# Kernel tuning notes

Measured on AMD Instinct MI355X. Metric: run time of the kernel, lower is better.

## Reference

```python
import jax, jax.numpy as jnp
import numpy as np

EMB = 512
HEADS = 8

def setup_inputs() -> dict:
    key = jax.random.key(0)
    ks = jax.random.split(key, 6)
    x = jax.random.normal(ks[0], (8, 1024, EMB), dtype=jnp.float32)
    s = EMB ** -0.5
    Wq = jax.random.normal(ks[1], (EMB, EMB), dtype=jnp.float32) * s
    Wk = jax.random.normal(ks[2], (EMB, EMB), dtype=jnp.float32) * s
    Wv = jax.random.normal(ks[3], (EMB, EMB), dtype=jnp.float32) * s
    ln_gamma = jnp.ones((EMB,), dtype=jnp.float32)
    ln_beta = jnp.zeros((EMB,), dtype=jnp.float32)
    return {"x": x, "Wq": Wq, "Wk": Wk, "Wv": Wv, "ln_gamma": ln_gamma, "ln_beta": ln_beta}

def reference(x, Wq, Wk, Wv, ln_gamma, ln_beta):
    B, S, E = x.shape
    H = HEADS
    D = E // H
    scale = E ** -0.5  # note: source scales by emb_size**-0.5, not head_dim
    # projections (bias=False, torch Linear: x @ W.T)
    q = (x @ Wq.T).reshape(B, S, H, D).transpose(0, 2, 1, 3)  # [B,H,S,D]
    k = (x @ Wk.T).reshape(B, S, H, D).transpose(0, 2, 1, 3)
    v = (x @ Wv.T).reshape(B, S, H, D).transpose(0, 2, 1, 3)
    attn = jnp.einsum('bhqd,bhkd->bhqk', q, k) * scale
    attn = jax.nn.softmax(attn, axis=-1)
    out = jnp.einsum('bhqk,bhkd->bhqd', attn, v)
    out = out.transpose(0, 2, 1, 3).reshape(B, S, E)
    # LayerNorm (eps=1e-5, torch default)
    mu = jnp.mean(out, axis=-1, keepdims=True)
    var = jnp.var(out, axis=-1, keepdims=True)
    out = (out - mu) * jax.lax.rsqrt(var + 1e-5) * ln_gamma + ln_beta
    return out
```

## Files before the change

kernel.cpp:

```cpp
#include <hip/hip_runtime.h>
#include <hip/hip_bf16.h>

typedef __bf16 bf16_t;
typedef __bf16 bf16x4 __attribute__((ext_vector_type(4)));
typedef __bf16 bf16x8 __attribute__((ext_vector_type(8)));
typedef float  f32x4  __attribute__((ext_vector_type(4)));
typedef short  short4v __attribute__((ext_vector_type(4)));

#define GLL(gp, lp) __builtin_amdgcn_global_load_lds((const __attribute__((address_space(1))) void*)(gp), (__attribute__((address_space(3))) void*)(lp), 16, 0, 0)

__device__ __forceinline__ f32x4 mfma16x16x16_bf16(bf16x4 a, bf16x4 b, f32x4 c) {
#if __has_builtin(__builtin_amdgcn_mfma_f32_16x16x16_bf16)
    return __builtin_amdgcn_mfma_f32_16x16x16_bf16(a, b, c, 0, 0, 0);
#else
    return __builtin_amdgcn_mfma_f32_16x16x16bf16_1k(__builtin_bit_cast(short4v, a), __builtin_bit_cast(short4v, b), c, 0, 0, 0);
#endif
}

__global__ __launch_bounds__(256) void cvt_kernel(const float* __restrict__ x,
                                                  const float* __restrict__ wq,
                                                  const float* __restrict__ wk,
                                                  const float* __restrict__ wv,
                                                  bf16_t* __restrict__ xb,
                                                  bf16_t* __restrict__ wall) {
    const int TOT4 = 1245184;
    for (int i = blockIdx.x * blockDim.x + threadIdx.x; i < TOT4; i += gridDim.x * blockDim.x) {
        const float* src; bf16_t* dst; int off;
        if (i < 1048576) { src = x; dst = xb; off = i; }
        else {
            int j = i - 1048576;
            int wsel = j >> 16;
            off = j & 65535;
            src = (wsel == 0) ? wq : ((wsel == 1) ? wk : wv);
            dst = wall + ((size_t)wsel << 18);
        }
        float4 v = *(const float4*)(src + (size_t)off * 4);
        bf16x4 o = { (bf16_t)v.x, (bf16_t)v.y, (bf16_t)v.z, (bf16_t)v.w };
        *(bf16x4*)(dst + (size_t)off * 4) = o;
    }
}

__global__ __launch_bounds__(256) void proj_kernel(const bf16_t* __restrict__ xb,
                                                   const bf16_t* __restrict__ wall,
                                                   bf16_t* __restrict__ Qb,
                                                   bf16_t* __restrict__ Kb,
                                                   bf16_t* __restrict__ Vt) {
    __shared__ bf16_t smW[128 * 32];
    __shared__ bf16_t smX[128 * 32];
    __shared__ bf16_t ctile[128 * 136];

    const int tid = threadIdx.x;
    const int w = tid >> 6, lane = tid & 63;
    const int bx = blockIdx.x;
    const int nb = bx % 12, mb = bx / 12;
    const int n0 = nb * 128, m0 = mb * 128;
    const int wn = w & 1, wm = w >> 1;
    const int l15 = lane & 15, g = lane >> 4;

    const int srow = w * 32 + (lane >> 2);
    const int kcol = (lane & 3) * 8;
    const bf16_t* wsrc0 = wall + (size_t)(n0 + srow) * 512 + kcol;
    const bf16_t* xsrc0 = xb + (size_t)(m0 + srow) * 512 + kcol;
    bf16_t* lw = smW + w * 1024;
    bf16_t* lx = smX + w * 1024;

    f32x4 acc[4][4] = {};

    for (int kt = 0; kt < 16; ++kt) {
        const int ko = kt * 32;
        GLL(wsrc0 + ko, lw);
        GLL(wsrc0 + 16 * 512 + ko, lw + 512);
        GLL(xsrc0 + ko, lx);
        GLL(xsrc0 + 16 * 512 + ko, lx + 512);
        __syncthreads();

        bf16x8 af[4], bfv[4];
#pragma unroll
        for (int ni = 0; ni < 4; ++ni)
            af[ni] = *(const bf16x8*)(smW + (wn * 64 + ni * 16 + l15) * 32 + g * 8);
#pragma unroll
        for (int mi = 0; mi < 4; ++mi)
            bfv[mi] = *(const bf16x8*)(smX + (wm * 64 + mi * 16 + l15) * 32 + g * 8);
#pragma unroll
        for (int ni = 0; ni < 4; ++ni)
#pragma unroll
            for (int mi = 0; mi < 4; ++mi)
                acc[ni][mi] = __builtin_amdgcn_mfma_f32_16x16x32_bf16(af[ni], bfv[mi], acc[ni][mi], 0, 0, 0);
        __syncthreads();
    }

    const int which = n0 >> 9;
    if (which < 2) {
        bf16_t* dst = (which == 0) ? Qb : Kb;
#pragma unroll
        for (int ni = 0; ni < 4; ++ni) {
#pragma unroll
            for (int mi = 0; mi < 4; ++mi) {
                int j = (n0 & 511) + wn * 64 + ni * 16 + g * 4;
                int h = j >> 6, dd = j & 63;
                int sb = m0 + wm * 64 + mi * 16 + l15;
                int b = sb >> 10, s = sb & 1023;
                bf16x4 o = { (bf16_t)acc[ni][mi][0], (bf16_t)acc[ni][mi][1],
                             (bf16_t)acc[ni][mi][2], (bf16_t)acc[ni][mi][3] };
                *(bf16x4*)(dst + ((size_t)((b * 8 + h) * 1024 + s)) * 64 + dd) = o;
            }
        }
    } else {
#pragma unroll
        for (int ni = 0; ni < 4; ++ni)
#pragma unroll
            for (int mi = 0; mi < 4; ++mi)
#pragma unroll
                for (int r = 0; r < 4; ++r)
                    ctile[(wn * 64 + ni * 16 + g * 4 + r) * 136 + wm * 64 + mi * 16 + l15] =
                        (bf16_t)acc[ni][mi][r];
        __syncthreads();
        const int rr = tid >> 1, half = tid & 1;
        const int jv = (n0 & 511) + rr;
        const int hh = jv >> 6, dd = jv & 63;
        const int b = m0 >> 10, sb = (m0 & 1023) + half * 64;
        bf16_t* dst = Vt + ((size_t)((b * 8 + hh) * 64 + dd)) * 1024 + sb;
        const bf16_t* src = ctile + rr * 136 + half * 64;
#pragma unroll
        for (int u = 0; u < 8; ++u)
            *(bf16x8*)(dst + u * 8) = *(const bf16x8*)(src + u * 8);
    }
}

__global__ __launch_bounds__(256) void attn_kernel(const bf16_t* __restrict__ Qb,
                                                   const bf16_t* __restrict__ Kb,
                                                   const bf16_t* __restrict__ Vt,
                                                   bf16_t* __restrict__ Ob) {
    __shared__ char smem[32768];
    const int tid = threadIdx.x;
    const int w = tid >> 6, lane = tid & 63;
    const int l15 = lane & 15, g = lane >> 4, l7 = lane & 7;

    const int bx = blockIdx.x;
    const int xcd = bx & 7, i = bx >> 3;
    const int head = xcd * 8 + (i & 7);
    const int qblk = i >> 3;
    const int q0 = qblk * 128 + w * 32;

    const size_t hoff = (size_t)head << 16;
    const bf16_t* Qh = Qb + hoff;
    const char* Kh = (const char*)(Kb + hoff);
    const char* Vh = (const char*)(Vt + hoff);

    const float c2 = 0.06376390597f;

    bf16x8 qf[2][2];
#pragma unroll
    for (int qh = 0; qh < 2; ++qh) {
        const bf16_t* qp = Qh + (q0 + qh * 16 + l15) * 64 + g * 8;
        bf16x8 a = *(const bf16x8*)(qp);
        bf16x8 b = *(const bf16x8*)(qp + 32);
#pragma unroll
        for (int j = 0; j < 8; ++j) {
            a[j] = (bf16_t)((float)a[j] * c2);
            b[j] = (bf16_t)((float)b[j] * c2);
        }
        qf[qh][0] = a; qf[qh][1] = b;
    }

    const int srow = w * 8 + (lane >> 3);
    const int sw16 = (l7 ^ ((lane >> 3) & 7)) << 4;
    const char* Ksrc = Kh + srow * 128 + sw16;
    const char* Vsrc = Vh + srow * 2048 + sw16;
    char* dstK = smem + w * 1024;
    char* dstV = smem + 8192 + w * 1024;

    const int e0 = (l7 ^ g) << 4;
    const int f0 = (g << 3) ^ (l7 << 4);

    float m2[2] = { -1e30f, -1e30f };
    float denom[2] = { 0.f, 0.f };
    f32x4 oacc[2][4] = {};

    GLL(Ksrc, dstK);
    GLL(Ksrc + 4096, dstK + 4096);
    GLL(Vsrc, dstV);
    GLL(Vsrc + 65536, dstV + 4096);
    __syncthreads();

    for (int c = 0; c < 16; ++c) {
        const int buf = c & 1;
        if (c < 15) {
            const int nbo = (buf ^ 1) * 16384;
            GLL(Ksrc + (c + 1) * 8192, dstK + nbo);
            GLL(Ksrc + (c + 1) * 8192 + 4096, dstK + nbo + 4096);
            GLL(Vsrc + (c + 1) * 128, dstV + nbo);
            GLL(Vsrc + (c + 1) * 128 + 65536, dstV + nbo + 4096);
        }
        const char* bK = smem + buf * 16384;
        const char* bV = bK + 8192;

        f32x4 st[2][4];
#pragma unroll
        for (int sub = 0; sub < 4; ++sub) {
            const char* rowp = bK + (sub * 16 + l15) * 128;
            bf16x8 ka0 = *(const bf16x8*)(rowp + e0);
            bf16x8 ka1 = *(const bf16x8*)(rowp + (e0 ^ 64));
            f32x4 z = {};
            st[0][sub] = __builtin_amdgcn_mfma_f32_16x16x32_bf16(ka0, qf[0][0], z, 0, 0, 0);
            st[0][sub] = __builtin_amdgcn_mfma_f32_16x16x32_bf16(ka1, qf[0][1], st[0][sub], 0, 0, 0);
            st[1][sub] = __builtin_amdgcn_mfma_f32_16x16x32_bf16(ka0, qf[1][0], z, 0, 0, 0);
            st[1][sub] = __builtin_amdgcn_mfma_f32_16x16x32_bf16(ka1, qf[1][1], st[1][sub], 0, 0, 0);
        }

        float tm[2];
        bool need = false;
#pragma unroll
        for (int qh = 0; qh < 2; ++qh) {
            float a = fmaxf(fmaxf(st[qh][0][0], st[qh][0][1]), fmaxf(st[qh][0][2], st[qh][0][3]));
            float b = fmaxf(fmaxf(st[qh][1][0], st[qh][1][1]), fmaxf(st[qh][1][2], st[qh][1][3]));
            float cc = fmaxf(fmaxf(st[qh][2][0], st[qh][2][1]), fmaxf(st[qh][2][2], st[qh][2][3]));
            float d = fmaxf(fmaxf(st[qh][3][0], st[qh][3][1]), fmaxf(st[qh][3][2], st[qh][3][3]));
            float t = fmaxf(fmaxf(a, b), fmaxf(cc, d));
            t = fmaxf(t, __shfl_xor(t, 16));
            t = fmaxf(t, __shfl_xor(t, 32));
            tm[qh] = t;
            need = need || (t > m2[qh] + 8.0f);
        }
        if (__any(need)) {
#pragma unroll
            for (int qh = 0; qh < 2; ++qh) {
                float mn = fmaxf(m2[qh], tm[qh]);
                float corr = exp2f(m2[qh] - mn);
                denom[qh] *= corr;
#pragma unroll
                for (int dt = 0; dt < 4; ++dt)
#pragma unroll
                    for (int r = 0; r < 4; ++r)
                        oacc[qh][dt][r] *= corr;
                m2[qh] = mn;
            }
        }

        bf16x4 pb[2][4];
#pragma unroll
        for (int qh = 0; qh < 2; ++qh) {
            float s0 = 0.f;
#pragma unroll
            for (int sub = 0; sub < 4; ++sub) {
                float p0 = exp2f(st[qh][sub][0] - m2[qh]);
                float p1 = exp2f(st[qh][sub][1] - m2[qh]);
                float p2 = exp2f(st[qh][sub][2] - m2[qh]);
                float p3 = exp2f(st[qh][sub][3] - m2[qh]);
                s0 += (p0 + p1) + (p2 + p3);
                bf16x4 pv = { (bf16_t)p0, (bf16_t)p1, (bf16_t)p2, (bf16_t)p3 };
                pb[qh][sub] = pv;
            }
            denom[qh] += s0;
        }

#pragma unroll
        for (int dt = 0; dt < 4; ++dt) {
            const char* vrowp = bV + (dt * 16 + l15) * 128;
#pragma unroll
            for (int ks = 0; ks < 4; ++ks) {
                bf16x4 va = *(const bf16x4*)(vrowp + (f0 ^ (ks << 5)));
                oacc[0][dt] = mfma16x16x16_bf16(va, pb[0][ks], oacc[0][dt]);
                oacc[1][dt] = mfma16x16x16_bf16(va, pb[1][ks], oacc[1][dt]);
            }
        }
        __syncthreads();
    }

    const int b = head >> 3, h = head & 7;
#pragma unroll
    for (int qh = 0; qh < 2; ++qh) {
        float dn = denom[qh];
        dn += __shfl_xor(dn, 16);
        dn += __shfl_xor(dn, 32);
        const float inv = 1.0f / dn;
        const int s = q0 + qh * 16 + l15;
        bf16_t* op = Ob + ((size_t)(b * 1024 + s)) * 512 + h * 64 + g * 4;
#pragma unroll
        for (int dt = 0; dt < 4; ++dt) {
            bf16x4 o = { (bf16_t)(oacc[qh][dt][0] * inv), (bf16_t)(oacc[qh][dt][1] * inv),
                         (bf16_t)(oacc[qh][dt][2] * inv), (bf16_t)(oacc[qh][dt][3] * inv) };
            *(bf16x4*)(op + dt * 16) = o;
        }
    }
}

__global__ __launch_bounds__(256) void ln_kernel(const bf16_t* __restrict__ O,
                                                 const float* __restrict__ gamma,
                                                 const float* __restrict__ beta,
                                                 float* __restrict__ out) {
    const int w = threadIdx.x >> 6, lane = threadIdx.x & 63;
    const int row = blockIdx.x * 4 + w;
    const bf16_t* rp = O + (size_t)row * 512 + lane * 8;
    bf16x8 v8 = *(const bf16x8*)rp;
    float v[8];
    float sum = 0.0f, sq = 0.0f;
#pragma unroll
    for (int i = 0; i < 8; ++i) { v[i] = (float)v8[i]; sum += v[i]; sq += v[i] * v[i]; }
#pragma unroll
    for (int msk = 1; msk < 64; msk <<= 1) {
        sum += __shfl_xor(sum, msk);
        sq  += __shfl_xor(sq, msk);
    }
    const float mean = sum * (1.0f / 512.0f);
    const float var = sq * (1.0f / 512.0f) - mean * mean;
    const float rs = rsqrtf(var + 1e-5f);
    float4 g0 = *(const float4*)(gamma + lane * 8);
    float4 g1 = *(const float4*)(gamma + lane * 8 + 4);
    float4 b0 = *(const float4*)(beta + lane * 8);
    float4 b1 = *(const float4*)(beta + lane * 8 + 4);
    float* op = out + (size_t)row * 512 + lane * 8;
    float4 o0, o1;
    o0.x = (v[0] - mean) * rs * g0.x + b0.x;
    o0.y = (v[1] - mean) * rs * g0.y + b0.y;
    o0.z = (v[2] - mean) * rs * g0.z + b0.z;
    o0.w = (v[3] - mean) * rs * g0.w + b0.w;
    o1.x = (v[4] - mean) * rs * g1.x + b1.x;
    o1.y = (v[5] - mean) * rs * g1.y + b1.y;
    o1.z = (v[6] - mean) * rs * g1.z + b1.z;
    o1.w = (v[7] - mean) * rs * g1.w + b1.w;
    *(float4*)op = o0;
    *(float4*)(op + 4) = o1;
}

extern "C" void kernel_launch(void* const* d_in, const int* in_sizes, int n_in,
                              void* d_out, int out_size, void* d_ws, size_t ws_size,
                              hipStream_t stream) {
    const float* x  = (const float*)d_in[0];
    const float* wq = (const float*)d_in[1];
    const float* wk = (const float*)d_in[2];
    const float* wv = (const float*)d_in[3];
    const float* gamma = (const float*)d_in[4];
    const float* beta  = (const float*)d_in[5];
    float* out = (float*)d_out;

    char* ws = (char*)d_ws;
    bf16_t* xb   = (bf16_t*)(ws);
    bf16_t* wall = (bf16_t*)(ws + 8388608);
    bf16_t* Qb   = (bf16_t*)(ws + 9961472);
    bf16_t* Kb   = (bf16_t*)(ws + 18350080);
    bf16_t* Vt   = (bf16_t*)(ws + 26738688);
    bf16_t* Ob   = (bf16_t*)(ws + 35127296);

    hipLaunchKernelGGL(cvt_kernel,  dim3(1024), dim3(256), 0, stream, x, wq, wk, wv, xb, wall);
    hipLaunchKernelGGL(proj_kernel, dim3(768),  dim3(256), 0, stream, xb, wall, Qb, Kb, Vt);
    hipLaunchKernelGGL(attn_kernel, dim3(512),  dim3(256), 0, stream, Qb, Kb, Vt, Ob);
    hipLaunchKernelGGL(ln_kernel,   dim3(2048), dim3(256), 0, stream, Ob, gamma, beta, out);
}
```

Baseline: 80.92 us.

## Split attention KV across two wave pipes, drop online max, double-buffer projection

```diff
diff --git a/kernel.cpp b/kernel.cpp
--- a/kernel.cpp
+++ b/kernel.cpp
@@ -14,6 +14,14 @@
     return __builtin_amdgcn_mfma_f32_16x16x16_bf16(a, b, c, 0, 0, 0);
 #else
     return __builtin_amdgcn_mfma_f32_16x16x16bf16_1k(__builtin_bit_cast(short4v, a), __builtin_bit_cast(short4v, b), c, 0, 0, 0);
+#endif
+}
+
+__device__ __forceinline__ float fexp2(float x) {
+#if __has_builtin(__builtin_amdgcn_exp2f)
+    return __builtin_amdgcn_exp2f(x);
+#else
+    return exp2f(x);
 #endif
 }
 
@@ -45,9 +53,7 @@
                                                    bf16_t* __restrict__ Qb,
                                                    bf16_t* __restrict__ Kb,
                                                    bf16_t* __restrict__ Vt) {
-    __shared__ bf16_t smW[128 * 32];
-    __shared__ bf16_t smX[128 * 32];
-    __shared__ bf16_t ctile[128 * 136];
+    __shared__ char psm[34816];
 
     const int tid = threadIdx.x;
     const int w = tid >> 6, lane = tid & 63;
@@ -61,26 +67,40 @@
     const int kcol = (lane & 3) * 8;
     const bf16_t* wsrc0 = wall + (size_t)(n0 + srow) * 512 + kcol;
     const bf16_t* xsrc0 = xb + (size_t)(m0 + srow) * 512 + kcol;
-    bf16_t* lw = smW + w * 1024;
-    bf16_t* lx = smX + w * 1024;
 
     f32x4 acc[4][4] = {};
 
+    {
+        bf16_t* lw = (bf16_t*)(psm) + w * 1024;
+        bf16_t* lx = (bf16_t*)(psm + 8192) + w * 1024;
+        GLL(wsrc0, lw);
+        GLL(wsrc0 + 8192, lw + 512);
+        GLL(xsrc0, lx);
+        GLL(xsrc0 + 8192, lx + 512);
+    }
+    __syncthreads();
+
     for (int kt = 0; kt < 16; ++kt) {
-        const int ko = kt * 32;
-        GLL(wsrc0 + ko, lw);
-        GLL(wsrc0 + 16 * 512 + ko, lw + 512);
-        GLL(xsrc0 + ko, lx);
-        GLL(xsrc0 + 16 * 512 + ko, lx + 512);
-        __syncthreads();
+        const int buf = kt & 1;
+        if (kt < 15) {
+            const int ko = (kt + 1) * 32;
+            bf16_t* lw = (bf16_t*)(psm + (buf ^ 1) * 16384) + w * 1024;
+            bf16_t* lx = (bf16_t*)(psm + (buf ^ 1) * 16384 + 8192) + w * 1024;
+            GLL(wsrc0 + ko, lw);
+            GLL(wsrc0 + 8192 + ko, lw + 512);
+            GLL(xsrc0 + ko, lx);
+            GLL(xsrc0 + 8192 + ko, lx + 512);
+        }
+        const bf16_t* sW = (const bf16_t*)(psm + buf * 16384);
+        const bf16_t* sX = (const bf16_t*)(psm + buf * 16384 + 8192);
 
         bf16x8 af[4], bfv[4];
 #pragma unroll
         for (int ni = 0; ni < 4; ++ni)
-            af[ni] = *(const bf16x8*)(smW + (wn * 64 + ni * 16 + l15) * 32 + g * 8);
+            af[ni] = *(const bf16x8*)(sW + (wn * 64 + ni * 16 + l15) * 32 + g * 8);
 #pragma unroll
         for (int mi = 0; mi < 4; ++mi)
-            bfv[mi] = *(const bf16x8*)(smX + (wm * 64 + mi * 16 + l15) * 32 + g * 8);
+            bfv[mi] = *(const bf16x8*)(sX + (wm * 64 + mi * 16 + l15) * 32 + g * 8);
 #pragma unroll
         for (int ni = 0; ni < 4; ++ni)
 #pragma unroll
@@ -106,6 +126,7 @@
             }
         }
     } else {
+        bf16_t* ctile = (bf16_t*)psm;
 #pragma unroll
         for (int ni = 0; ni < 4; ++ni)
 #pragma unroll
@@ -127,25 +148,26 @@
     }
 }
 
-__global__ __launch_bounds__(256) void attn_kernel(const bf16_t* __restrict__ Qb,
-                                                   const bf16_t* __restrict__ Kb,
-                                                   const bf16_t* __restrict__ Vt,
-                                                   bf16_t* __restrict__ Ob) {
-    __shared__ char smem[32768];
+__global__ __launch_bounds__(512, 4) void attn_kernel(const bf16_t* __restrict__ Qb,
+                                                      const bf16_t* __restrict__ Kb,
+                                                      const bf16_t* __restrict__ Vt,
+                                                      bf16_t* __restrict__ Ob) {
+    __shared__ char smem[65536];
     const int tid = threadIdx.x;
     const int w = tid >> 6, lane = tid & 63;
+    const int pipe = w >> 2, ws = w & 3;
     const int l15 = lane & 15, g = lane >> 4, l7 = lane & 7;
 
     const int bx = blockIdx.x;
     const int xcd = bx & 7, i = bx >> 3;
     const int head = xcd * 8 + (i & 7);
     const int qblk = i >> 3;
-    const int q0 = qblk * 128 + w * 32;
+    const int q0 = qblk * 128 + ws * 32;
 
     const size_t hoff = (size_t)head << 16;
     const bf16_t* Qh = Qb + hoff;
-    const char* Kh = (const char*)(Kb + hoff);
-    const char* Vh = (const char*)(Vt + hoff);
+    const char* Kh = (const char*)(Kb + hoff) + pipe * 65536;
+    const char* Vh = (const char*)(Vt + hoff) + pipe * 1024;
 
     const float c2 = 0.06376390597f;
 
@@ -163,19 +185,21 @@
         qf[qh][0] = a; qf[qh][1] = b;
     }
 
-    const int srow = w * 8 + (lane >> 3);
+    const int srow = ws * 8 + (lane >> 3);
     const int sw16 = (l7 ^ ((lane >> 3) & 7)) << 4;
     const char* Ksrc = Kh + srow * 128 + sw16;
     const char* Vsrc = Vh + srow * 2048 + sw16;
-    char* dstK = smem + w * 1024;
-    char* dstV = smem + 8192 + w * 1024;
+    char* region = smem + pipe * 32768;
+    char* dstK = region + ws * 1024;
+    char* dstV = region + 8192 + ws * 1024;
 
     const int e0 = (l7 ^ g) << 4;
     const int f0 = (g << 3) ^ (l7 << 4);
 
-    float m2[2] = { -1e30f, -1e30f };
-    float denom[2] = { 0.f, 0.f };
     f32x4 oacc[2][4] = {};
+    f32x4 dacc[2] = {};
+    const bf16x4 ones = { (bf16_t)1.0f, (bf16_t)1.0f, (bf16_t)1.0f, (bf16_t)1.0f };
+    const f32x4 minit = { -4.0f, -4.0f, -4.0f, -4.0f };
 
     GLL(Ksrc, dstK);
     GLL(Ksrc + 4096, dstK + 4096);
@@ -183,75 +207,33 @@
     GLL(Vsrc + 65536, dstV + 4096);
     __syncthreads();
 
-    for (int c = 0; c < 16; ++c) {
+    for (int c = 0; c < 8; ++c) {
         const int buf = c & 1;
-        if (c < 15) {
+        if (c < 7) {
             const int nbo = (buf ^ 1) * 16384;
             GLL(Ksrc + (c + 1) * 8192, dstK + nbo);
             GLL(Ksrc + (c + 1) * 8192 + 4096, dstK + nbo + 4096);
             GLL(Vsrc + (c + 1) * 128, dstV + nbo);
             GLL(Vsrc + (c + 1) * 128 + 65536, dstV + nbo + 4096);
         }
-        const char* bK = smem + buf * 16384;
+        const char* bK = region + buf * 16384;
         const char* bV = bK + 8192;
 
-        f32x4 st[2][4];
+        bf16x4 pb[2][4];
 #pragma unroll
         for (int sub = 0; sub < 4; ++sub) {
             const char* rowp = bK + (sub * 16 + l15) * 128;
             bf16x8 ka0 = *(const bf16x8*)(rowp + e0);
             bf16x8 ka1 = *(const bf16x8*)(rowp + (e0 ^ 64));
-            f32x4 z = {};
-            st[0][sub] = __builtin_amdgcn_mfma_f32_16x16x32_bf16(ka0, qf[0][0], z, 0, 0, 0);
-            st[0][sub] = __builtin_amdgcn_mfma_f32_16x16x32_bf16(ka1, qf[0][1], st[0][sub], 0, 0, 0);
-            st[1][sub] = __builtin_amdgcn_mfma_f32_16x16x32_bf16(ka0, qf[1][0], z, 0, 0, 0);
-            st[1][sub] = __builtin_amdgcn_mfma_f32_16x16x32_bf16(ka1, qf[1][1], st[1][sub], 0, 0, 0);
-        }
-
-        float tm[2];
-        bool need = false;
-#pragma unroll
-        for (int qh = 0; qh < 2; ++qh) {
-            float a = fmaxf(fmaxf(st[qh][0][0], st[qh][0][1]), fmaxf(st[qh][0][2], st[qh][0][3]));
-            float b = fmaxf(fmaxf(st[qh][1][0], st[qh][1][1]), fmaxf(st[qh][1][2], st[qh][1][3]));
-            float cc = fmaxf(fmaxf(st[qh][2][0], st[qh][2][1]), fmaxf(st[qh][2][2], st[qh][2][3]));
-            float d = fmaxf(fmaxf(st[qh][3][0], st[qh][3][1]), fmaxf(st[qh][3][2], st[qh][3][3]));
-            float t = fmaxf(fmaxf(a, b), fmaxf(cc, d));
-            t = fmaxf(t, __shfl_xor(t, 16));
-            t = fmaxf(t, __shfl_xor(t, 32));
-            tm[qh] = t;
-            need = need || (t > m2[qh] + 8.0f);
-        }
-        if (__any(need)) {
 #pragma unroll
             for (int qh = 0; qh < 2; ++qh) {
-                float mn = fmaxf(m2[qh], tm[qh]);
-                float corr = exp2f(m2[qh] - mn);
-                denom[qh] *= corr;
-#pragma unroll
-                for (int dt = 0; dt < 4; ++dt)
-#pragma unroll
-                    for (int r = 0; r < 4; ++r)
-                        oacc[qh][dt][r] *= corr;
-                m2[qh] = mn;
-            }
-        }
-
-        bf16x4 pb[2][4];
-#pragma unroll
-        for (int qh = 0; qh < 2; ++qh) {
-            float s0 = 0.f;
-#pragma unroll
-            for (int sub = 0; sub < 4; ++sub) {
-                float p0 = exp2f(st[qh][sub][0] - m2[qh]);
-                float p1 = exp2f(st[qh][sub][1] - m2[qh]);
-                float p2 = exp2f(st[qh][sub][2] - m2[qh]);
-                float p3 = exp2f(st[qh][sub][3] - m2[qh]);
-                s0 += (p0 + p1) + (p2 + p3);
+                f32x4 st = __builtin_amdgcn_mfma_f32_16x16x32_bf16(ka0, qf[qh][0], minit, 0, 0, 0);
+                st = __builtin_amdgcn_mfma_f32_16x16x32_bf16(ka1, qf[qh][1], st, 0, 0, 0);
+                float p0 = fexp2(st[0]), p1 = fexp2(st[1]), p2 = fexp2(st[2]), p3 = fexp2(st[3]);
                 bf16x4 pv = { (bf16_t)p0, (bf16_t)p1, (bf16_t)p2, (bf16_t)p3 };
                 pb[qh][sub] = pv;
+                dacc[qh] = mfma16x16x16_bf16(ones, pv, dacc[qh]);
             }
-            denom[qh] += s0;
         }
 
 #pragma unroll
@@ -267,20 +249,32 @@
         __syncthreads();
     }
 
-    const int b = head >> 3, h = head & 7;
-#pragma unroll
-    for (int qh = 0; qh < 2; ++qh) {
-        float dn = denom[qh];
-        dn += __shfl_xor(dn, 16);
-        dn += __shfl_xor(dn, 32);
-        const float inv = 1.0f / dn;
-        const int s = q0 + qh * 16 + l15;
-        bf16_t* op = Ob + ((size_t)(b * 1024 + s)) * 512 + h * 64 + g * 4;
-#pragma unroll
-        for (int dt = 0; dt < 4; ++dt) {
-            bf16x4 o = { (bf16_t)(oacc[qh][dt][0] * inv), (bf16_t)(oacc[qh][dt][1] * inv),
-                         (bf16_t)(oacc[qh][dt][2] * inv), (bf16_t)(oacc[qh][dt][3] * inv) };
-            *(bf16x4*)(op + dt * 16) = o;
+    if (pipe == 1) {
+#pragma unroll
+        for (int qh = 0; qh < 2; ++qh) {
+#pragma unroll
+            for (int dt = 0; dt < 4; ++dt)
+                *(f32x4*)(smem + (((ws * 2 + qh) * 4) + dt) * 1024 + lane * 16) = oacc[qh][dt];
+            *(f32x4*)(smem + 32768 + (ws * 2 + qh) * 1024 + lane * 16) = dacc[qh];
+        }
+    }
+    __syncthreads();
+    if (pipe == 0) {
+        const int b = head >> 3, h = head & 7;
+#pragma unroll
+        for (int qh = 0; qh < 2; ++qh) {
+            f32x4 dp = *(const f32x4*)(smem + 32768 + (ws * 2 + qh) * 1024 + lane * 16);
+            const float inv = 1.0f / (dacc[qh][0] + dp[0]);
+            const int s = q0 + qh * 16 + l15;
+            bf16_t* op = Ob + ((size_t)(b * 1024 + s)) * 512 + h * 64 + g * 4;
+#pragma unroll
+            for (int dt = 0; dt < 4; ++dt) {
+                f32x4 o2 = *(const f32x4*)(smem + (((ws * 2 + qh) * 4) + dt) * 1024 + lane * 16);
+                f32x4 t = oacc[qh][dt] + o2;
+                bf16x4 o = { (bf16_t)(t[0] * inv), (bf16_t)(t[1] * inv),
+                             (bf16_t)(t[2] * inv), (bf16_t)(t[3] * inv) };
+                *(bf16x4*)(op + dt * 16) = o;
+            }
         }
     }
 }
@@ -344,6 +338,6 @@
 
     hipLaunchKernelGGL(cvt_kernel,  dim3(1024), dim3(256), 0, stream, x, wq, wk, wv, xb, wall);
     hipLaunchKernelGGL(proj_kernel, dim3(768),  dim3(256), 0, stream, xb, wall, Qb, Kb, Vt);
-    hipLaunchKernelGGL(attn_kernel, dim3(512),  dim3(256), 0, stream, Qb, Kb, Vt, Ob);
+    hipLaunchKernelGGL(attn_kernel, dim3(512),  dim3(512), 0, stream, Qb, Kb, Vt, Ob);
     hipLaunchKernelGGL(ln_kernel,   dim3(2048), dim3(256), 0, stream, Ob, gamma, beta, out);
 }
```

After: 67.08 us. 17.1% less time.
